# Kernel optimization log

Measured on AMD Instinct MI355X. Metric: run time of the kernel, lower is better.

## Reference

```python
import jax, jax.numpy as jnp
import numpy as np

B, I, NN, D = 4, 128, 127, 128   # batch, n_index, nodes without super node, hidden
N = NN + 1                        # nodes including super node
H, L, FFN = 4, 4, 32              # heads, layers, ffn dim
DK = D // H // 2                  # att_size = 16 per head, per stream
SCALE = DK ** -0.5


def layernorm(x, g, b, eps=1e-5):
    m = jnp.mean(x, -1, keepdims=True)
    v = jnp.mean((x - m) ** 2, -1, keepdims=True)
    return (x - m) * jax.lax.rsqrt(v + eps) * g + b


def mha(x, bias, ln_g, ln_b, wq, bq, wk, bk, wv, bv):
    # EncoderLayerSimple: pre-LN then MHA with additive bias, no out-proj (enable_out_layer=False)
    y = layernorm(x, ln_g, ln_b)
    Bx, S, _ = y.shape
    q = (y @ wq.T + bq).reshape(Bx, S, H, DK) * SCALE
    k = (y @ wk.T + bk).reshape(Bx, S, H, DK)
    v = (y @ wv.T + bv).reshape(Bx, S, H, DK)
    s = jnp.einsum('bihd,bjhd->bhij', q, k) + bias
    a = jax.nn.softmax(s, axis=-1)
    return jnp.einsum('bhij,bjhd->bihd', a, v).reshape(Bx, S, H * DK)


def setup_inputs():
    ks = jax.random.split(jax.random.key(0), 24)
    f = jnp.float32
    inp = {
        'node_embedded': jax.random.normal(ks[0], (B, I, NN, D), f),
        'heights': jax.random.normal(ks[1], (B, I, NN, D), f),
        'rel_pos_mat': jax.random.randint(ks[2], (B, I, N, N), 0, 192),
        'tree_attn_bias': jax.random.normal(ks[3], (B, I, N, N), f) * 0.1,
        'index_attn_bias': jax.random.normal(ks[4], (B, N, I, I), f) * 0.1,
        'super_node_emb': jax.random.normal(ks[5], (1, D), f) * 0.02,
        'rel_pos_emb': (jax.random.normal(ks[6], (192, H), f) * 0.02).at[0].set(0.0),  # padding_idx=0
        'super_dist': jax.random.normal(ks[7], (1, H), f) * 0.02,
        'attn_out_w': jax.random.normal(ks[8], (D, D), f) * 0.02,
        'attn_out_b': jnp.zeros((D,), f),
        'ffn_ln_g': jnp.ones((D,), f), 'ffn_ln_b': jnp.zeros((D,), f),
        'ffn_w1': jax.random.normal(ks[9], (FFN, D), f) * 0.02,
        'ffn_b1': jnp.zeros((FFN,), f),
        'ffn_w2': jax.random.normal(ks[10], (D, FFN), f) * 0.02,
        'ffn_b2': jnp.zeros((D,), f),
        'final_ln_g': jnp.ones((D,), f), 'final_ln_b': jnp.zeros((D,), f),
    }
    for pre, base in (('enc1', 11), ('enc2', 17)):
        inp[pre + '_ln_g'] = jnp.ones((L, D), f)
        inp[pre + '_ln_b'] = jnp.zeros((L, D), f)
        for j, nm in enumerate(('wq', 'wk', 'wv')):
            inp[pre + '_' + nm] = jax.random.normal(ks[base + j], (L, H * DK, D), f) * 0.02
            inp[pre + '_b' + nm[1]] = jnp.zeros((L, H * DK), f)
    return inp


def reference(node_embedded, heights, rel_pos_mat, tree_attn_bias, index_attn_bias,
              super_node_emb, rel_pos_emb, super_dist, attn_out_w, attn_out_b,
              ffn_ln_g, ffn_ln_b, ffn_w1, ffn_b1, ffn_w2, ffn_b2, final_ln_g, final_ln_b,
              enc1_ln_g, enc1_ln_b, enc1_wq, enc1_bq, enc1_wk, enc1_bk, enc1_wv, enc1_bv,
              enc2_ln_g, enc2_ln_b, enc2_wq, enc2_bq, enc2_wk, enc2_bk, enc2_wv, enc2_bv):
    node = node_embedded + heights
    sup = jnp.broadcast_to(super_node_emb.reshape(1, 1, 1, D), (B, I, 1, D))
    x = jnp.concatenate([sup, node], axis=2)  # [B, I, N, D]
    # tree attention bias: per-head repeat + rel-pos embedding gather + super-node distance
    rel = rel_pos_emb[rel_pos_mat.reshape(B * I, N, N)]            # [BI, N, N, H]
    tab = tree_attn_bias.reshape(B * I, N, N)[:, None] + jnp.transpose(rel, (0, 3, 1, 2))
    t = super_dist.reshape(1, H, 1)
    tab = tab.at[:, :, 1:, 0].add(t)
    tab = tab.at[:, :, 0, :].add(t)                                # [BI, H, N, N]
    iab = index_attn_bias.reshape(B * N, I, I)[:, None]            # [BN, 1, I, I] (broadcast over heads)
    for l in range(L):
        x1 = jnp.transpose(x, (0, 2, 1, 3)).reshape(B * N, I, D)   # index-axis stream
        x2 = x.reshape(B * I, N, D)                                # node-axis stream
        y1 = mha(x1, iab, enc1_ln_g[l], enc1_ln_b[l], enc1_wq[l], enc1_bq[l],
                 enc1_wk[l], enc1_bk[l], enc1_wv[l], enc1_bv[l])
        y2 = mha(x2, tab, enc2_ln_g[l], enc2_ln_b[l], enc2_wq[l], enc2_bq[l],
                 enc2_wk[l], enc2_bk[l], enc2_wv[l], enc2_bv[l])
        y1 = jnp.transpose(y1.reshape(B, N, I, D // 2), (0, 2, 1, 3))
        y2 = y2.reshape(B, I, N, D // 2)
        y = jnp.concatenate([y1, y2], axis=-1) @ attn_out_w.T + attn_out_b
        x = x + y
        z = layernorm(x, ffn_ln_g, ffn_ln_b)
        z = jax.nn.gelu(z @ ffn_w1.T + ffn_b1, approximate=False) @ ffn_w2.T + ffn_b2
        x = x + z
    return layernorm(x, final_ln_g, final_ln_b)
```

## Files before the change

kernel.cpp:

```cpp
#include <hip/hip_runtime.h>
#include <cstdint>
#include <cstddef>


__device__ __forceinline__ int swz (int r, int c){ return c ^ (((r >> 2) & 7) << 2); }
__device__ __forceinline__ int swzA(int r, int c){ return c ^ ((r & 7) << 2); }

__global__ __launch_bounds__(256) void k_build_x(const float4* __restrict__ ne,
    const float4* __restrict__ hts, const float4* __restrict__ sup,
    float4* __restrict__ X){
  int idx = blockIdx.x * 256 + threadIdx.x;
  int d4 = idx & 31;
  int n  = (idx >> 5) & 127;
  int bi = idx >> 12;
  float4 v;
  if (n == 0){
    v = sup[d4];
  } else {
    size_t s = ((size_t)bi * 127 + (n - 1)) * 32 + d4;
    float4 a = ne[s], h = hts[s];
    v.x = a.x + h.x; v.y = a.y + h.y; v.z = a.z + h.z; v.w = a.w + h.w;
  }
  X[idx] = v;
}

struct QkvArgs {
  const float* x;
  const float* ln_g[2]; const float* ln_b[2];
  const float* w[6];  const float* wb[6];
  float* out[6];
};

__global__ __launch_bounds__(256, 3) void k_qkv(QkvArgs A){
  __shared__ float sY[32 * 128];
  __shared__ float sW[64 * 128];
  const int r0  = blockIdx.x * 32;
  const int enc = blockIdx.y;
  const int t   = threadIdx.x;
  {
    const float4* xs = (const float4*)(A.x + (size_t)r0 * 128);
    #pragma unroll
    for (int it = 0; it < 4; ++it){
      int el = it * 256 + t;
      int rr = el >> 5, c4 = (el & 31) * 4;
      *(float4*)&sY[rr * 128 + swzA(rr, c4)] = xs[el];
    }
  }
  __syncthreads();
  const int row = t >> 3, part = t & 7;
  float s1 = 0.f, s2 = 0.f;
  float4 xv[4];
  #pragma unroll
  for (int q = 0; q < 4; ++q){
    int c4 = part * 16 + q * 4;
    xv[q] = *(const float4*)&sY[row * 128 + swzA(row, c4)];
    s1 += xv[q].x + xv[q].y + xv[q].z + xv[q].w;
    s2 += xv[q].x*xv[q].x + xv[q].y*xv[q].y + xv[q].z*xv[q].z + xv[q].w*xv[q].w;
  }
  s1 += __shfl_xor(s1, 1); s2 += __shfl_xor(s2, 1);
  s1 += __shfl_xor(s1, 2); s2 += __shfl_xor(s2, 2);
  s1 += __shfl_xor(s1, 4); s2 += __shfl_xor(s2, 4);
  float mean = s1 * (1.f / 128.f);
  float rstd = rsqrtf(s2 * (1.f / 128.f) - mean * mean + 1e-5f);
  {
    const float* lg = A.ln_g[enc];
    const float* lb = A.ln_b[enc];
    #pragma unroll
    for (int q = 0; q < 4; ++q){
      int cc = part * 16 + q * 4;
      int a  = row * 128 + swzA(row, cc);
      float4 gv = *(const float4*)&lg[cc];
      float4 bv = *(const float4*)&lb[cc];
      float4 y;
      y.x = (xv[q].x - mean) * rstd * gv.x + bv.x;
      y.y = (xv[q].y - mean) * rstd * gv.y + bv.y;
      y.z = (xv[q].z - mean) * rstd * gv.z + bv.z;
      y.w = (xv[q].w - mean) * rstd * gv.w + bv.w;
      *(float4*)&sY[a] = y;
    }
  }
  const int tc = t & 15, tr = t >> 4;
  const int kb_x  = (tc & 7) << 2;
  const int ra0 = tr * 2, ra1 = tr * 2 + 1;
  const int ka_x0 = (ra0 & 7) << 2;
  const int ka_x1 = (ra1 & 7) << 2;
  for (int g3 = 0; g3 < 3; ++g3){
    const int g = enc * 3 + g3;
    __syncthreads();
    {
      const float4* wsrc = (const float4*)A.w[g];
      #pragma unroll
      for (int it = 0; it < 8; ++it){
        int el = it * 256 + t;
        int rr = el >> 5, c4 = (el & 31) * 4;
        *(float4*)&sW[rr * 128 + swz(rr, c4)] = wsrc[el];
      }
    }
    __syncthreads();
    float acc[2][4] = {};
    #pragma unroll
    for (int k = 0; k < 128; k += 4){
      float4 av[2], bv[4];
      av[0] = *(const float4*)&sY[ra0 * 128 + (k ^ ka_x0)];
      av[1] = *(const float4*)&sY[ra1 * 128 + (k ^ ka_x1)];
      int kb = k ^ kb_x;
      #pragma unroll
      for (int q = 0; q < 4; ++q) bv[q] = *(const float4*)&sW[(tc * 4 + q) * 128 + kb];
      #pragma unroll
      for (int i2 = 0; i2 < 2; ++i2)
        #pragma unroll
        for (int j2 = 0; j2 < 4; ++j2){
          acc[i2][j2] += av[i2].x * bv[j2].x;
          acc[i2][j2] += av[i2].y * bv[j2].y;
          acc[i2][j2] += av[i2].z * bv[j2].z;
          acc[i2][j2] += av[i2].w * bv[j2].w;
        }
    }
    const float scale = (g3 == 0) ? 0.25f : 1.0f;
    const float* wb = A.wb[g];
    const float b0 = wb[tc*4], b1 = wb[tc*4+1], b2 = wb[tc*4+2], b3 = wb[tc*4+3];
    float* outp = A.out[g];
    const int h_ = tc >> 2, u_ = (tc & 3) * 4;
    #pragma unroll
    for (int i2 = 0; i2 < 2; ++i2){
      int gr = r0 + tr * 2 + i2;
      size_t off = ((size_t)((gr >> 7) * 4 + h_)) * 2048 + (gr & 127) * 16 + u_;
      float4 o;
      o.x = (acc[i2][0] + b0) * scale;
      o.y = (acc[i2][1] + b1) * scale;
      o.z = (acc[i2][2] + b2) * scale;
      o.w = (acc[i2][3] + b3) * scale;
      *(float4*)&outp[off] = o;
    }
  }
}

__global__ __launch_bounds__(512, 4) void k_attn1(const float* __restrict__ Q,
    const float* __restrict__ K, const float* __restrict__ V,
    const float* __restrict__ iab, float* __restrict__ YC){
  __shared__ float sK[128][16];
  __shared__ float sV[128][16];
  const int seq = blockIdx.x;
  const int h   = blockIdx.y;
  const int t   = threadIdx.x;
  const int i   = t >> 2, qd = t & 3;
  const int b_ = seq >> 7, n_ = seq & 127;
  const size_t rbase = ((size_t)((b_ * 128 + i) * 4 + h)) * 2048 + n_ * 16;
  {
    int swc = (qd * 4) ^ ((i >> 5) << 2);
    *(float4*)&sK[i][swc] = *(const float4*)&K[rbase + qd * 4];
    *(float4*)&sV[i][swc] = *(const float4*)&V[rbase + qd * 4];
  }
  float q[16];
  #pragma unroll
  for (int u = 0; u < 4; ++u){
    float4 v = *(const float4*)&Q[rbase + u * 4];
    q[u*4+0] = v.x; q[u*4+1] = v.y; q[u*4+2] = v.z; q[u*4+3] = v.w;
  }
  __syncthreads();
  const float4* brow = (const float4*)(iab + (size_t)seq * 16384 + (size_t)i * 128 + qd * 32);
  const int jsw = qd << 2;
  float s[32];
  #pragma unroll
  for (int j8 = 0; j8 < 8; ++j8){
    float4 bv4 = brow[j8];
    float bb[4] = {bv4.x, bv4.y, bv4.z, bv4.w};
    #pragma unroll
    for (int u = 0; u < 4; ++u){
      int jj = j8 * 4 + u;
      int j  = qd * 32 + jj;
      float acc = bb[u];
      #pragma unroll
      for (int u4 = 0; u4 < 4; ++u4){
        float4 kv = *(const float4*)&sK[j][(u4 * 4) ^ jsw];
        acc += q[u4*4+0]*kv.x + q[u4*4+1]*kv.y + q[u4*4+2]*kv.z + q[u4*4+3]*kv.w;
      }
      s[jj] = acc;
    }
  }
  float m = -1e30f;
  #pragma unroll
  for (int jj = 0; jj < 32; ++jj) m = fmaxf(m, s[jj]);
  m = fmaxf(m, __shfl_xor(m, 1));
  m = fmaxf(m, __shfl_xor(m, 2));
  float sum = 0.f;
  #pragma unroll
  for (int jj = 0; jj < 32; ++jj){ float ev = __expf(s[jj] - m); s[jj] = ev; sum += ev; }
  sum += __shfl_xor(sum, 1);
  sum += __shfl_xor(sum, 2);
  float inv = 1.f / sum;
  float o[16] = {};
  #pragma unroll
  for (int jj = 0; jj < 32; ++jj){
    int j = qd * 32 + jj;
    float p = s[jj];
    #pragma unroll
    for (int u4 = 0; u4 < 4; ++u4){
      float4 vv = *(const float4*)&sV[j][(u4 * 4) ^ jsw];
      o[u4*4+0] += p * vv.x; o[u4*4+1] += p * vv.y;
      o[u4*4+2] += p * vv.z; o[u4*4+3] += p * vv.w;
    }
  }
  #pragma unroll
  for (int e = 0; e < 16; ++e){
    o[e] += __shfl_xor(o[e], 1);
    o[e] += __shfl_xor(o[e], 2);
  }
  size_t off = (((size_t)(b_ * 128 + i)) * 128 + n_) * 128 + h * 16 + qd * 4;
  float4 v;
  v.x = o[qd*4+0]*inv; v.y = o[qd*4+1]*inv; v.z = o[qd*4+2]*inv; v.w = o[qd*4+3]*inv;
  *(float4*)&YC[off] = v;
}

__global__ __launch_bounds__(512, 4) void k_attn2(const float* __restrict__ Q,
    const float* __restrict__ K, const float* __restrict__ V,
    const float* __restrict__ tree, const int* __restrict__ mat,
    const float* __restrict__ relemb, const float* __restrict__ sdist,
    float* __restrict__ YC){
  __shared__ float sK[128][16];
  __shared__ float sV[128][16];
  __shared__ float srel[768];
  const int seq = blockIdx.x;
  const int h   = blockIdx.y;
  const int t   = threadIdx.x;
  const int i   = t >> 2, qd = t & 3;
  const size_t base = ((size_t)(seq * 4 + h)) * 2048;
  {
    int swc = (qd * 4) ^ ((i >> 5) << 2);
    *(float4*)&sK[i][swc] = *(const float4*)&K[base + i * 16 + qd * 4];
    *(float4*)&sV[i][swc] = *(const float4*)&V[base + i * 16 + qd * 4];
  }
  float q[16];
  #pragma unroll
  for (int u = 0; u < 4; ++u){
    float4 v = *(const float4*)&Q[base + i * 16 + u * 4];
    q[u*4+0] = v.x; q[u*4+1] = v.y; q[u*4+2] = v.z; q[u*4+3] = v.w;
  }
  for (int u = t; u < 768; u += 512) srel[u] = relemb[u];
  const float tsup = sdist[h];
  __syncthreads();
  const float4* trow = (const float4*)(tree + (size_t)seq * 16384 + (size_t)i * 128 + qd * 32);
  const int4*   mrow = (const int4*)(mat + (size_t)seq * 16384 + (size_t)i * 128 + qd * 32);
  const int jsw = qd << 2;
  float s[32];
  #pragma unroll
  for (int j8 = 0; j8 < 8; ++j8){
    float4 tv = trow[j8];
    int4  mv  = mrow[j8];
    float bb[4];
    bb[0] = tv.x + srel[mv.x * 4 + h];
    bb[1] = tv.y + srel[mv.y * 4 + h];
    bb[2] = tv.z + srel[mv.z * 4 + h];
    bb[3] = tv.w + srel[mv.w * 4 + h];
    #pragma unroll
    for (int u = 0; u < 4; ++u){
      int jj = j8 * 4 + u;
      int j  = qd * 32 + jj;
      float acc = bb[u];
      if (i == 0) acc += tsup;
      else if (j == 0) acc += tsup;
      #pragma unroll
      for (int u4 = 0; u4 < 4; ++u4){
        float4 kv = *(const float4*)&sK[j][(u4 * 4) ^ jsw];
        acc += q[u4*4+0]*kv.x + q[u4*4+1]*kv.y + q[u4*4+2]*kv.z + q[u4*4+3]*kv.w;
      }
      s[jj] = acc;
    }
  }
  float m = -1e30f;
  #pragma unroll
  for (int jj = 0; jj < 32; ++jj) m = fmaxf(m, s[jj]);
  m = fmaxf(m, __shfl_xor(m, 1));
  m = fmaxf(m, __shfl_xor(m, 2));
  float sum = 0.f;
  #pragma unroll
  for (int jj = 0; jj < 32; ++jj){ float ev = __expf(s[jj] - m); s[jj] = ev; sum += ev; }
  sum += __shfl_xor(sum, 1);
  sum += __shfl_xor(sum, 2);
  float inv = 1.f / sum;
  float o[16] = {};
  #pragma unroll
  for (int jj = 0; jj < 32; ++jj){
    int j = qd * 32 + jj;
    float p = s[jj];
    #pragma unroll
    for (int u4 = 0; u4 < 4; ++u4){
      float4 vv = *(const float4*)&sV[j][(u4 * 4) ^ jsw];
      o[u4*4+0] += p * vv.x; o[u4*4+1] += p * vv.y;
      o[u4*4+2] += p * vv.z; o[u4*4+3] += p * vv.w;
    }
  }
  #pragma unroll
  for (int e = 0; e < 16; ++e){
    o[e] += __shfl_xor(o[e], 1);
    o[e] += __shfl_xor(o[e], 2);
  }
  size_t off = (((size_t)seq) * 128 + i) * 128 + 64 + h * 16 + qd * 4;
  float4 v;
  v.x = o[qd*4+0]*inv; v.y = o[qd*4+1]*inv; v.z = o[qd*4+2]*inv; v.w = o[qd*4+3]*inv;
  *(float4*)&YC[off] = v;
}

__global__ __launch_bounds__(256, 2) void k_attn_out(const float* __restrict__ YC,
    const float* __restrict__ W, const float* __restrict__ bias, float* __restrict__ X){
  __shared__ float sA[64 * 128];
  __shared__ float sW[64 * 128];
  const int r0 = blockIdx.x * 64, c0 = blockIdx.y * 64;
  const int t  = threadIdx.x;
  {
    const float4* as   = (const float4*)(YC + (size_t)r0 * 128);
    const float4* wsrc = (const float4*)(W + (size_t)c0 * 128);
    #pragma unroll
    for (int it = 0; it < 8; ++it){
      int e  = it * 256 + t;
      int rr = e >> 5, c4 = (e & 31) * 4;
      int cs = swz(rr, c4);
      *(float4*)&sA[rr * 128 + cs] = as[e];
      *(float4*)&sW[rr * 128 + cs] = wsrc[e];
    }
  }
  __syncthreads();
  const int tc = t & 15, tr = t >> 4;
  float acc[4][4] = {};
  #pragma unroll
  for (int k = 0; k < 128; k += 4){
    float4 av[4], bv[4];
    int ka = k ^ ((tr & 7) << 2);
    int kb = k ^ ((tc & 7) << 2);
    #pragma unroll
    for (int q = 0; q < 4; ++q) av[q] = *(const float4*)&sA[(tr * 4 + q) * 128 + ka];
    #pragma unroll
    for (int q = 0; q < 4; ++q) bv[q] = *(const float4*)&sW[(tc * 4 + q) * 128 + kb];
    #pragma unroll
    for (int i2 = 0; i2 < 4; ++i2)
      #pragma unroll
      for (int j2 = 0; j2 < 4; ++j2){
        acc[i2][j2] += av[i2].x * bv[j2].x;
        acc[i2][j2] += av[i2].y * bv[j2].y;
        acc[i2][j2] += av[i2].z * bv[j2].z;
        acc[i2][j2] += av[i2].w * bv[j2].w;
      }
  }
  const float b0 = bias[c0 + tc*4], b1 = bias[c0 + tc*4 + 1],
              b2 = bias[c0 + tc*4 + 2], b3 = bias[c0 + tc*4 + 3];
  #pragma unroll
  for (int i2 = 0; i2 < 4; ++i2){
    int r = r0 + tr * 4 + i2;
    float4* xp = (float4*)&X[(size_t)r * 128 + c0 + tc * 4];
    float4 xv = *xp;
    xv.x += acc[i2][0] + b0;
    xv.y += acc[i2][1] + b1;
    xv.z += acc[i2][2] + b2;
    xv.w += acc[i2][3] + b3;
    *xp = xv;
  }
}

__global__ __launch_bounds__(256, 2) void k_ffn(float* __restrict__ X,
    const float* __restrict__ lg, const float* __restrict__ lb,
    const float* __restrict__ W1, const float* __restrict__ b1,
    const float* __restrict__ W2, const float* __restrict__ b2){
  __shared__ float sW1[32][132];
  __shared__ float sW2[128][36];
  __shared__ float sY[16][132];
  __shared__ float sH[16][33];
  const int t  = threadIdx.x;
  const int r0 = blockIdx.x * 16;
  {
    const float4* w1s = (const float4*)W1;
    #pragma unroll
    for (int it = 0; it < 4; ++it){
      int e = it * 256 + t;
      int r = e >> 5, c4 = (e & 31) * 4;
      *(float4*)&sW1[r][c4] = w1s[e];
    }
    const float4* w2s = (const float4*)W2;
    #pragma unroll
    for (int it = 0; it < 4; ++it){
      int e = it * 256 + t;
      int r = e >> 3, c4 = (e & 7) * 4;
      *(float4*)&sW2[r][c4] = w2s[e];
    }
  }
  const int row = t >> 4, p = t & 15;
  const size_t gb = ((size_t)(r0 + row)) * 128;
  float4 xa = *(const float4*)&X[gb + p * 8];
  float4 xb = *(const float4*)&X[gb + p * 8 + 4];
  float s1 = xa.x + xa.y + xa.z + xa.w + xb.x + xb.y + xb.z + xb.w;
  float s2 = xa.x*xa.x + xa.y*xa.y + xa.z*xa.z + xa.w*xa.w
           + xb.x*xb.x + xb.y*xb.y + xb.z*xb.z + xb.w*xb.w;
  #pragma unroll
  for (int msk = 1; msk < 16; msk <<= 1){ s1 += __shfl_xor(s1, msk); s2 += __shfl_xor(s2, msk); }
  float mean = s1 * (1.f / 128.f);
  float rstd = rsqrtf(s2 * (1.f / 128.f) - mean * mean + 1e-5f);
  {
    float4 g0 = *(const float4*)&lg[p * 8], g1 = *(const float4*)&lg[p * 8 + 4];
    float4 c0 = *(const float4*)&lb[p * 8], c1 = *(const float4*)&lb[p * 8 + 4];
    float4 y0, y1;
    y0.x = (xa.x-mean)*rstd*g0.x + c0.x;  y0.y = (xa.y-mean)*rstd*g0.y + c0.y;
    y0.z = (xa.z-mean)*rstd*g0.z + c0.z;  y0.w = (xa.w-mean)*rstd*g0.w + c0.w;
    y1.x = (xb.x-mean)*rstd*g1.x + c1.x;  y1.y = (xb.y-mean)*rstd*g1.y + c1.y;
    y1.z = (xb.z-mean)*rstd*g1.z + c1.z;  y1.w = (xb.w-mean)*rstd*g1.w + c1.w;
    *(float4*)&sY[row][p * 8]     = y0;
    *(float4*)&sY[row][p * 8 + 4] = y1;
  }
  __syncthreads();
  #pragma unroll
  for (int cc = 0; cc < 2; ++cc){
    int c = p + cc * 16;
    float acc = b1[c];
    #pragma unroll
    for (int k = 0; k < 128; ++k) acc += sY[row][k] * sW1[c][k];
    sH[row][c] = 0.5f * acc * (1.0f + erff(acc * 0.70710678118654752f));
  }
  __syncthreads();
  #pragma unroll
  for (int u = 0; u < 8; ++u){
    int c = p + u * 16;
    float acc = b2[c];
    #pragma unroll
    for (int k = 0; k < 32; ++k) acc += sH[row][k] * sW2[c][k];
    X[gb + c] += acc;
  }
}

__global__ __launch_bounds__(256) void k_final(const float* __restrict__ X,
    const float* __restrict__ g, const float* __restrict__ b, float* __restrict__ out){
  const int t = threadIdx.x;
  const int row = blockIdx.x * 64 + (t >> 2), p = t & 3;
  const float* src = X + (size_t)row * 128 + p * 32;
  float4 v[8];
  float s1 = 0.f, s2 = 0.f;
  #pragma unroll
  for (int u = 0; u < 8; ++u){
    v[u] = *(const float4*)&src[u * 4];
    s1 += v[u].x + v[u].y + v[u].z + v[u].w;
    s2 += v[u].x*v[u].x + v[u].y*v[u].y + v[u].z*v[u].z + v[u].w*v[u].w;
  }
  s1 += __shfl_xor(s1, 1); s2 += __shfl_xor(s2, 1);
  s1 += __shfl_xor(s1, 2); s2 += __shfl_xor(s2, 2);
  float mean = s1 * (1.f / 128.f);
  float rstd = rsqrtf(s2 * (1.f / 128.f) - mean * mean + 1e-5f);
  float* dst = out + (size_t)row * 128 + p * 32;
  #pragma unroll
  for (int u = 0; u < 8; ++u){
    int c = p * 32 + u * 4;
    float4 gv = *(const float4*)&g[c];
    float4 bv = *(const float4*)&b[c];
    float4 o;
    o.x = (v[u].x - mean) * rstd * gv.x + bv.x;
    o.y = (v[u].y - mean) * rstd * gv.y + bv.y;
    o.z = (v[u].z - mean) * rstd * gv.z + bv.z;
    o.w = (v[u].w - mean) * rstd * gv.w + bv.w;
    *(float4*)&dst[u * 4] = o;
  }
}

extern "C" void kernel_launch(void* const* d_in, const int* in_sizes, int n_in,
                              void* d_out, int out_size, void* d_ws, size_t ws_size,
                              hipStream_t stream){
  (void)in_sizes; (void)n_in; (void)out_size; (void)ws_size;
  const float* node_embedded   = (const float*)d_in[0];
  const float* heights         = (const float*)d_in[1];
  const int*   rel_pos_mat     = (const int*)d_in[2];
  const float* tree_attn_bias  = (const float*)d_in[3];
  const float* index_attn_bias = (const float*)d_in[4];
  const float* super_node_emb  = (const float*)d_in[5];
  const float* rel_pos_emb     = (const float*)d_in[6];
  const float* super_dist      = (const float*)d_in[7];
  const float* attn_out_w      = (const float*)d_in[8];
  const float* attn_out_b      = (const float*)d_in[9];
  const float* ffn_ln_g        = (const float*)d_in[10];
  const float* ffn_ln_b        = (const float*)d_in[11];
  const float* ffn_w1          = (const float*)d_in[12];
  const float* ffn_b1          = (const float*)d_in[13];
  const float* ffn_w2          = (const float*)d_in[14];
  const float* ffn_b2          = (const float*)d_in[15];
  const float* final_ln_g      = (const float*)d_in[16];
  const float* final_ln_b      = (const float*)d_in[17];
  const float* e1_ln_g = (const float*)d_in[18];
  const float* e1_ln_b = (const float*)d_in[19];
  const float* e1_wq   = (const float*)d_in[20];
  const float* e1_bq   = (const float*)d_in[21];
  const float* e1_wk   = (const float*)d_in[22];
  const float* e1_bk   = (const float*)d_in[23];
  const float* e1_wv   = (const float*)d_in[24];
  const float* e1_bv   = (const float*)d_in[25];
  const float* e2_ln_g = (const float*)d_in[26];
  const float* e2_ln_b = (const float*)d_in[27];
  const float* e2_wq   = (const float*)d_in[28];
  const float* e2_bq   = (const float*)d_in[29];
  const float* e2_wk   = (const float*)d_in[30];
  const float* e2_bk   = (const float*)d_in[31];
  const float* e2_wv   = (const float*)d_in[32];
  const float* e2_bv   = (const float*)d_in[33];

  float* ws = (float*)d_ws;
  const size_t SZX = 8388608, SZH = 4194304;
  float* X  = ws;
  float* Q1 = X  + SZX;
  float* K1 = Q1 + SZH;
  float* V1 = K1 + SZH;
  float* Q2 = V1 + SZH;
  float* K2 = Q2 + SZH;
  float* V2 = K2 + SZH;
  float* YC = V2 + SZH;

  k_build_x<<<8192, 256, 0, stream>>>((const float4*)node_embedded, (const float4*)heights,
                                      (const float4*)super_node_emb, (float4*)X);
  for (int l = 0; l < 4; ++l){
    QkvArgs A;
    A.x = X;
    A.ln_g[0] = e1_ln_g + l * 128;  A.ln_b[0] = e1_ln_b + l * 128;
    A.ln_g[1] = e2_ln_g + l * 128;  A.ln_b[1] = e2_ln_b + l * 128;
    A.w[0] = e1_wq + (size_t)l * 8192;  A.wb[0] = e1_bq + l * 64;
    A.w[1] = e1_wk + (size_t)l * 8192;  A.wb[1] = e1_bk + l * 64;
    A.w[2] = e1_wv + (size_t)l * 8192;  A.wb[2] = e1_bv + l * 64;
    A.w[3] = e2_wq + (size_t)l * 8192;  A.wb[3] = e2_bq + l * 64;
    A.w[4] = e2_wk + (size_t)l * 8192;  A.wb[4] = e2_bk + l * 64;
    A.w[5] = e2_wv + (size_t)l * 8192;  A.wb[5] = e2_bv + l * 64;
    A.out[0] = Q1; A.out[1] = K1; A.out[2] = V1;
    A.out[3] = Q2; A.out[4] = K2; A.out[5] = V2;
    k_qkv<<<dim3(2048, 2), 256, 0, stream>>>(A);
    k_attn1<<<dim3(512, 4), 512, 0, stream>>>(Q1, K1, V1, index_attn_bias, YC);
    k_attn2<<<dim3(512, 4), 512, 0, stream>>>(Q2, K2, V2, tree_attn_bias, rel_pos_mat,
                                              rel_pos_emb, super_dist, YC);
    k_attn_out<<<dim3(1024, 2), 256, 0, stream>>>(YC, attn_out_w, attn_out_b, X);
    k_ffn<<<4096, 256, 0, stream>>>(X, ffn_ln_g, ffn_ln_b, ffn_w1, ffn_b1, ffn_w2, ffn_b2);
  }
  k_final<<<1024, 256, 0, stream>>>(X, final_ln_g, final_ln_b, (float*)d_out);
}
```

Before: 2.131 ms.

## Process all heads per block in attention kernels to reuse bias loads

Both attention kernels now launch one block per sequence and loop over the four heads inside, staging K and V for all heads in shared memory. The per-sequence bias rows (index bias, or tree bias plus relative-position indices) are then shared across heads instead of being fetched again by a separate block per head. This targets redundant global bias traffic, at the cost of a quarter as many blocks, four times the LDS per block, and a serial loop over heads.

```diff
diff --git a/kernel.cpp b/kernel.cpp
--- a/kernel.cpp
+++ b/kernel.cpp
@@ -135,170 +135,178 @@
   }
 }
 
-__global__ __launch_bounds__(512, 4) void k_attn1(const float* __restrict__ Q,
+__global__ __launch_bounds__(512) void k_attn1(const float* __restrict__ Q,
     const float* __restrict__ K, const float* __restrict__ V,
     const float* __restrict__ iab, float* __restrict__ YC){
-  __shared__ float sK[128][16];
-  __shared__ float sV[128][16];
+  __shared__ float sK[4][128][16];
+  __shared__ float sV[4][128][16];
   const int seq = blockIdx.x;
-  const int h   = blockIdx.y;
   const int t   = threadIdx.x;
   const int i   = t >> 2, qd = t & 3;
   const int b_ = seq >> 7, n_ = seq & 127;
-  const size_t rbase = ((size_t)((b_ * 128 + i) * 4 + h)) * 2048 + n_ * 16;
-  {
-    int swc = (qd * 4) ^ ((i >> 5) << 2);
-    *(float4*)&sK[i][swc] = *(const float4*)&K[rbase + qd * 4];
-    *(float4*)&sV[i][swc] = *(const float4*)&V[rbase + qd * 4];
-  }
-  float q[16];
-  #pragma unroll
-  for (int u = 0; u < 4; ++u){
-    float4 v = *(const float4*)&Q[rbase + u * 4];
-    q[u*4+0] = v.x; q[u*4+1] = v.y; q[u*4+2] = v.z; q[u*4+3] = v.w;
+  const int swc = (qd * 4) ^ ((i >> 5) << 2);
+  #pragma unroll
+  for (int h = 0; h < 4; ++h){
+    const size_t rb = ((size_t)((b_ * 128 + i) * 4 + h)) * 2048 + n_ * 16;
+    *(float4*)&sK[h][i][swc] = *(const float4*)&K[rb + qd * 4];
+    *(float4*)&sV[h][i][swc] = *(const float4*)&V[rb + qd * 4];
   }
   __syncthreads();
   const float4* brow = (const float4*)(iab + (size_t)seq * 16384 + (size_t)i * 128 + qd * 32);
   const int jsw = qd << 2;
-  float s[32];
-  #pragma unroll
-  for (int j8 = 0; j8 < 8; ++j8){
-    float4 bv4 = brow[j8];
-    float bb[4] = {bv4.x, bv4.y, bv4.z, bv4.w};
+  #pragma unroll 1
+  for (int h = 0; h < 4; ++h){
+    const size_t rb = ((size_t)((b_ * 128 + i) * 4 + h)) * 2048 + n_ * 16;
+    float q[16];
     #pragma unroll
     for (int u = 0; u < 4; ++u){
-      int jj = j8 * 4 + u;
-      int j  = qd * 32 + jj;
-      float acc = bb[u];
+      float4 v = *(const float4*)&Q[rb + u * 4];
+      q[u*4+0] = v.x; q[u*4+1] = v.y; q[u*4+2] = v.z; q[u*4+3] = v.w;
+    }
+    float s[32];
+    #pragma unroll
+    for (int j8 = 0; j8 < 8; ++j8){
+      float4 bv4 = brow[j8];
+      float bb[4] = {bv4.x, bv4.y, bv4.z, bv4.w};
+      #pragma unroll
+      for (int u = 0; u < 4; ++u){
+        int jj = j8 * 4 + u;
+        int j  = qd * 32 + jj;
+        float acc = bb[u];
+        #pragma unroll
+        for (int u4 = 0; u4 < 4; ++u4){
+          float4 kv = *(const float4*)&sK[h][j][(u4 * 4) ^ jsw];
+          acc += q[u4*4+0]*kv.x + q[u4*4+1]*kv.y + q[u4*4+2]*kv.z + q[u4*4+3]*kv.w;
+        }
+        s[jj] = acc;
+      }
+    }
+    float m = -1e30f;
+    #pragma unroll
+    for (int jj = 0; jj < 32; ++jj) m = fmaxf(m, s[jj]);
+    m = fmaxf(m, __shfl_xor(m, 1));
+    m = fmaxf(m, __shfl_xor(m, 2));
+    float sum = 0.f;
+    #pragma unroll
+    for (int jj = 0; jj < 32; ++jj){ float ev = __expf(s[jj] - m); s[jj] = ev; sum += ev; }
+    sum += __shfl_xor(sum, 1);
+    sum += __shfl_xor(sum, 2);
+    float inv = 1.f / sum;
+    float o[16] = {};
+    #pragma unroll
+    for (int jj = 0; jj < 32; ++jj){
+      int j = qd * 32 + jj;
+      float p = s[jj];
       #pragma unroll
       for (int u4 = 0; u4 < 4; ++u4){
-        float4 kv = *(const float4*)&sK[j][(u4 * 4) ^ jsw];
-        acc += q[u4*4+0]*kv.x + q[u4*4+1]*kv.y + q[u4*4+2]*kv.z + q[u4*4+3]*kv.w;
+        float4 vv = *(const float4*)&sV[h][j][(u4 * 4) ^ jsw];
+        o[u4*4+0] += p * vv.x; o[u4*4+1] += p * vv.y;
+        o[u4*4+2] += p * vv.z; o[u4*4+3] += p * vv.w;
       }
-      s[jj] = acc;
-    }
-  }
-  float m = -1e30f;
-  #pragma unroll
-  for (int jj = 0; jj < 32; ++jj) m = fmaxf(m, s[jj]);
-  m = fmaxf(m, __shfl_xor(m, 1));
-  m = fmaxf(m, __shfl_xor(m, 2));
-  float sum = 0.f;
-  #pragma unroll
-  for (int jj = 0; jj < 32; ++jj){ float ev = __expf(s[jj] - m); s[jj] = ev; sum += ev; }
-  sum += __shfl_xor(sum, 1);
-  sum += __shfl_xor(sum, 2);
-  float inv = 1.f / sum;
-  float o[16] = {};
-  #pragma unroll
-  for (int jj = 0; jj < 32; ++jj){
-    int j = qd * 32 + jj;
-    float p = s[jj];
-    #pragma unroll
-    for (int u4 = 0; u4 < 4; ++u4){
-      float4 vv = *(const float4*)&sV[j][(u4 * 4) ^ jsw];
-      o[u4*4+0] += p * vv.x; o[u4*4+1] += p * vv.y;
-      o[u4*4+2] += p * vv.z; o[u4*4+3] += p * vv.w;
-    }
-  }
-  #pragma unroll
-  for (int e = 0; e < 16; ++e){
-    o[e] += __shfl_xor(o[e], 1);
-    o[e] += __shfl_xor(o[e], 2);
-  }
-  size_t off = (((size_t)(b_ * 128 + i)) * 128 + n_) * 128 + h * 16 + qd * 4;
-  float4 v;
-  v.x = o[qd*4+0]*inv; v.y = o[qd*4+1]*inv; v.z = o[qd*4+2]*inv; v.w = o[qd*4+3]*inv;
-  *(float4*)&YC[off] = v;
-}
-
-__global__ __launch_bounds__(512, 4) void k_attn2(const float* __restrict__ Q,
+    }
+    #pragma unroll
+    for (int e = 0; e < 16; ++e){
+      o[e] += __shfl_xor(o[e], 1);
+      o[e] += __shfl_xor(o[e], 2);
+    }
+    size_t off = (((size_t)(b_ * 128 + i)) * 128 + n_) * 128 + h * 16 + qd * 4;
+    float4 v;
+    v.x = o[qd*4+0]*inv; v.y = o[qd*4+1]*inv; v.z = o[qd*4+2]*inv; v.w = o[qd*4+3]*inv;
+    *(float4*)&YC[off] = v;
+  }
+}
+
+__global__ __launch_bounds__(512) void k_attn2(const float* __restrict__ Q,
     const float* __restrict__ K, const float* __restrict__ V,
     const float* __restrict__ tree, const int* __restrict__ mat,
     const float* __restrict__ relemb, const float* __restrict__ sdist,
     float* __restrict__ YC){
-  __shared__ float sK[128][16];
-  __shared__ float sV[128][16];
+  __shared__ float sK[4][128][16];
+  __shared__ float sV[4][128][16];
   __shared__ float srel[768];
   const int seq = blockIdx.x;
-  const int h   = blockIdx.y;
   const int t   = threadIdx.x;
   const int i   = t >> 2, qd = t & 3;
-  const size_t base = ((size_t)(seq * 4 + h)) * 2048;
-  {
-    int swc = (qd * 4) ^ ((i >> 5) << 2);
-    *(float4*)&sK[i][swc] = *(const float4*)&K[base + i * 16 + qd * 4];
-    *(float4*)&sV[i][swc] = *(const float4*)&V[base + i * 16 + qd * 4];
-  }
-  float q[16];
-  #pragma unroll
-  for (int u = 0; u < 4; ++u){
-    float4 v = *(const float4*)&Q[base + i * 16 + u * 4];
-    q[u*4+0] = v.x; q[u*4+1] = v.y; q[u*4+2] = v.z; q[u*4+3] = v.w;
+  const int swc = (qd * 4) ^ ((i >> 5) << 2);
+  #pragma unroll
+  for (int h = 0; h < 4; ++h){
+    const size_t bh = ((size_t)(seq * 4 + h)) * 2048;
+    *(float4*)&sK[h][i][swc] = *(const float4*)&K[bh + i * 16 + qd * 4];
+    *(float4*)&sV[h][i][swc] = *(const float4*)&V[bh + i * 16 + qd * 4];
   }
   for (int u = t; u < 768; u += 512) srel[u] = relemb[u];
-  const float tsup = sdist[h];
   __syncthreads();
   const float4* trow = (const float4*)(tree + (size_t)seq * 16384 + (size_t)i * 128 + qd * 32);
   const int4*   mrow = (const int4*)(mat + (size_t)seq * 16384 + (size_t)i * 128 + qd * 32);
   const int jsw = qd << 2;
-  float s[32];
-  #pragma unroll
-  for (int j8 = 0; j8 < 8; ++j8){
-    float4 tv = trow[j8];
-    int4  mv  = mrow[j8];
-    float bb[4];
-    bb[0] = tv.x + srel[mv.x * 4 + h];
-    bb[1] = tv.y + srel[mv.y * 4 + h];
-    bb[2] = tv.z + srel[mv.z * 4 + h];
-    bb[3] = tv.w + srel[mv.w * 4 + h];
+  #pragma unroll 1
+  for (int h = 0; h < 4; ++h){
+    const size_t bh = ((size_t)(seq * 4 + h)) * 2048;
+    const float tsup = sdist[h];
+    float q[16];
     #pragma unroll
     for (int u = 0; u < 4; ++u){
-      int jj = j8 * 4 + u;
-      int j  = qd * 32 + jj;
-      float acc = bb[u];
-      if (i == 0) acc += tsup;
-      else if (j == 0) acc += tsup;
+      float4 v = *(const float4*)&Q[bh + i * 16 + u * 4];
+      q[u*4+0] = v.x; q[u*4+1] = v.y; q[u*4+2] = v.z; q[u*4+3] = v.w;
+    }
+    float s[32];
+    #pragma unroll
+    for (int j8 = 0; j8 < 8; ++j8){
+      float4 tv = trow[j8];
+      int4  mv  = mrow[j8];
+      float bb[4];
+      bb[0] = tv.x + srel[mv.x * 4 + h];
+      bb[1] = tv.y + srel[mv.y * 4 + h];
+      bb[2] = tv.z + srel[mv.z * 4 + h];
+      bb[3] = tv.w + srel[mv.w * 4 + h];
+      #pragma unroll
+      for (int u = 0; u < 4; ++u){
+        int jj = j8 * 4 + u;
+        int j  = qd * 32 + jj;
+        float acc = bb[u];
+        if (i == 0) acc += tsup;
+        else if (j == 0) acc += tsup;
+        #pragma unroll
+        for (int u4 = 0; u4 < 4; ++u4){
+          float4 kv = *(const float4*)&sK[h][j][(u4 * 4) ^ jsw];
+          acc += q[u4*4+0]*kv.x + q[u4*4+1]*kv.y + q[u4*4+2]*kv.z + q[u4*4+3]*kv.w;
+        }
+        s[jj] = acc;
+      }
+    }
+    float m = -1e30f;
+    #pragma unroll
+    for (int jj = 0; jj < 32; ++jj) m = fmaxf(m, s[jj]);
+    m = fmaxf(m, __shfl_xor(m, 1));
+    m = fmaxf(m, __shfl_xor(m, 2));
+    float sum = 0.f;
+    #pragma unroll
+    for (int jj = 0; jj < 32; ++jj){ float ev = __expf(s[jj] - m); s[jj] = ev; sum += ev; }
+    sum += __shfl_xor(sum, 1);
+    sum += __shfl_xor(sum, 2);
+    float inv = 1.f / sum;
+    float o[16] = {};
+    #pragma unroll
+    for (int jj = 0; jj < 32; ++jj){
+      int j = qd * 32 + jj;
+      float p = s[jj];
       #pragma unroll
       for (int u4 = 0; u4 < 4; ++u4){
-        float4 kv = *(const float4*)&sK[j][(u4 * 4) ^ jsw];
-        acc += q[u4*4+0]*kv.x + q[u4*4+1]*kv.y + q[u4*4+2]*kv.z + q[u4*4+3]*kv.w;
+        float4 vv = *(const float4*)&sV[h][j][(u4 * 4) ^ jsw];
+        o[u4*4+0] += p * vv.x; o[u4*4+1] += p * vv.y;
+        o[u4*4+2] += p * vv.z; o[u4*4+3] += p * vv.w;
       }
-      s[jj] = acc;
-    }
-  }
-  float m = -1e30f;
-  #pragma unroll
-  for (int jj = 0; jj < 32; ++jj) m = fmaxf(m, s[jj]);
-  m = fmaxf(m, __shfl_xor(m, 1));
-  m = fmaxf(m, __shfl_xor(m, 2));
-  float sum = 0.f;
-  #pragma unroll
-  for (int jj = 0; jj < 32; ++jj){ float ev = __expf(s[jj] - m); s[jj] = ev; sum += ev; }
-  sum += __shfl_xor(sum, 1);
-  sum += __shfl_xor(sum, 2);
-  float inv = 1.f / sum;
-  float o[16] = {};
-  #pragma unroll
-  for (int jj = 0; jj < 32; ++jj){
-    int j = qd * 32 + jj;
-    float p = s[jj];
-    #pragma unroll
-    for (int u4 = 0; u4 < 4; ++u4){
-      float4 vv = *(const float4*)&sV[j][(u4 * 4) ^ jsw];
-      o[u4*4+0] += p * vv.x; o[u4*4+1] += p * vv.y;
-      o[u4*4+2] += p * vv.z; o[u4*4+3] += p * vv.w;
-    }
-  }
-  #pragma unroll
-  for (int e = 0; e < 16; ++e){
-    o[e] += __shfl_xor(o[e], 1);
-    o[e] += __shfl_xor(o[e], 2);
-  }
-  size_t off = (((size_t)seq) * 128 + i) * 128 + 64 + h * 16 + qd * 4;
-  float4 v;
-  v.x = o[qd*4+0]*inv; v.y = o[qd*4+1]*inv; v.z = o[qd*4+2]*inv; v.w = o[qd*4+3]*inv;
-  *(float4*)&YC[off] = v;
+    }
+    #pragma unroll
+    for (int e = 0; e < 16; ++e){
+      o[e] += __shfl_xor(o[e], 1);
+      o[e] += __shfl_xor(o[e], 2);
+    }
+    size_t off = (((size_t)seq) * 128 + i) * 128 + 64 + h * 16 + qd * 4;
+    float4 v;
+    v.x = o[qd*4+0]*inv; v.y = o[qd*4+1]*inv; v.z = o[qd*4+2]*inv; v.w = o[qd*4+3]*inv;
+    *(float4*)&YC[off] = v;
+  }
 }
 
 __global__ __launch_bounds__(256, 2) void k_attn_out(const float* __restrict__ YC,
@@ -522,9 +530,9 @@
     A.out[0] = Q1; A.out[1] = K1; A.out[2] = V1;
     A.out[3] = Q2; A.out[4] = K2; A.out[5] = V2;
     k_qkv<<<dim3(2048, 2), 256, 0, stream>>>(A);
-    k_attn1<<<dim3(512, 4), 512, 0, stream>>>(Q1, K1, V1, index_attn_bias, YC);
-    k_attn2<<<dim3(512, 4), 512, 0, stream>>>(Q2, K2, V2, tree_attn_bias, rel_pos_mat,
-                                              rel_pos_emb, super_dist, YC);
+    k_attn1<<<512, 512, 0, stream>>>(Q1, K1, V1, index_attn_bias, YC);
+    k_attn2<<<512, 512, 0, stream>>>(Q2, K2, V2, tree_attn_bias, rel_pos_mat,
+                                     rel_pos_emb, super_dist, YC);
     k_attn_out<<<dim3(1024, 2), 256, 0, stream>>>(YC, attn_out_w, attn_out_b, X);
     k_ffn<<<4096, 256, 0, stream>>>(X, ffn_ln_g, ffn_ln_b, ffn_w1, ffn_b1, ffn_w2, ffn_b2);
   }
```

Measured after the change: 1.776 ms. -16.7%, faster.
